# Kernel tuning notes

Hardware: AMD Instinct MI355X
Metric: run time of the kernel (lower is better)

Reference implementation:

```python
import jax, jax.numpy as jnp
import numpy as np

D_MODEL = 1024
D_STATE = 64
D_CONV = 4
EXPAND = 2
HEADDIM = 64
FFN_MULT = 3
MEM_DIM = 256
D_INNER = EXPAND * D_MODEL            # 2048
NHEADS = D_INNER // HEADDIM           # 32
CONV_DIM = D_INNER + 2 * D_STATE      # x, B, C channels through the causal conv
D_IN_PROJ = 2 * D_INNER + 2 * D_STATE + NHEADS  # z, xBC, dt
FFN_HID = FFN_MULT * D_MODEL


def _rms(x, eps=1e-6):
    return x * jax.lax.rsqrt(jnp.mean(x * x, axis=-1, keepdims=True) + eps)


def _mamba2(u, in_proj_w, conv_w, conv_b, dt_bias, A_log, D_param, mnorm_w, out_proj_w):
    # u: [B, L, d_model]
    Bsz, L, _ = u.shape
    zxbcdt = u @ in_proj_w.T                                  # [B, L, D_IN_PROJ]
    z = zxbcdt[..., :D_INNER]                                 # gate branch
    xBC = zxbcdt[..., D_INNER:D_INNER + CONV_DIM]
    dt = zxbcdt[..., D_INNER + CONV_DIM:]                     # [B, L, H]
    # causal depthwise conv1d (kernel D_CONV) + silu
    xp = jnp.pad(xBC, ((0, 0), (D_CONV - 1, 0), (0, 0)))
    xBC = sum(xp[:, k:k + L, :] * conv_w[:, k] for k in range(D_CONV)) + conv_b
    xBC = jax.nn.silu(xBC)
    xh = xBC[..., :D_INNER].reshape(Bsz, L, NHEADS, HEADDIM)  # [B, L, H, P]
    Bm = xBC[..., D_INNER:D_INNER + D_STATE]                  # [B, L, N] (ngroups=1)
    Cm = xBC[..., D_INNER + D_STATE:]                         # [B, L, N]
    dt = jax.nn.softplus(dt + dt_bias)                        # [B, L, H]
    dA = jnp.exp(dt * (-jnp.exp(A_log)))                      # [B, L, H]

    def step(h, inp):
        # h: [B, H, P, N]
        da, dtt, xt, bt, ct = inp
        h = da[:, :, None, None] * h + jnp.einsum('bh,bhp,bn->bhpn', dtt, xt, bt)
        y = jnp.einsum('bhpn,bn->bhp', h, ct)
        return h, y

    h0 = jnp.zeros((Bsz, NHEADS, HEADDIM, D_STATE), u.dtype)
    xs = (jnp.moveaxis(dA, 1, 0), jnp.moveaxis(dt, 1, 0), jnp.moveaxis(xh, 1, 0),
          jnp.moveaxis(Bm, 1, 0), jnp.moveaxis(Cm, 1, 0))
    _, ys = jax.lax.scan(step, h0, xs)                        # ys: [L, B, H, P]
    y = jnp.moveaxis(ys, 0, 1) + D_param[None, None, :, None] * xh
    y = y.reshape(Bsz, L, D_INNER)
    y = _rms(y * jax.nn.silu(z)) * mnorm_w                    # RMSNormGated
    return y @ out_proj_w.T


def setup_inputs() -> dict:
    key = jax.random.key(0)
    ks = jax.random.split(key, 12)
    B, L = 1, 2048
    s = 0.02
    return {
        'x': jax.random.normal(ks[0], (B, L, D_MODEL), jnp.float32),
        'x0': jax.random.normal(ks[1], (B, L, D_MODEL), jnp.float32),
        'mem': jax.random.normal(ks[2], (B, MEM_DIM), jnp.float32),
        'resid_mix': jnp.stack([jnp.ones(D_MODEL), jnp.zeros(D_MODEL)]),
        'ssm_scale': jnp.ones(D_MODEL),
        'mlp_scale': jnp.ones(D_MODEL),
        'ssm_norm_w': jnp.ones(D_MODEL),
        'ffn_norm_w': jnp.ones(D_MODEL),
        'in_proj_w': jax.random.normal(ks[3], (D_IN_PROJ, D_MODEL), jnp.float32) * s,
        'conv_w': jax.random.normal(ks[4], (CONV_DIM, D_CONV), jnp.float32) * 0.2,
        'conv_b': jnp.zeros(CONV_DIM),
        'dt_bias': jax.random.uniform(ks[5], (NHEADS,), jnp.float32, -2.0, 0.0),
        'A_log': jnp.log(jnp.linspace(1.0, 16.0, NHEADS).astype(jnp.float32)),
        'D_param': jnp.ones(NHEADS),
        'mnorm_w': jnp.ones(D_INNER),
        'out_proj_w': jax.random.normal(ks[6], (D_MODEL, D_INNER), jnp.float32) * s,
        'gate_up_w': jax.random.normal(ks[7], (2 * FFN_HID, D_MODEL), jnp.float32) * s,
        'down_w': jax.random.normal(ks[8], (D_MODEL, FFN_HID), jnp.float32) * s,
    }


def reference(x, x0, mem, resid_mix, ssm_scale, mlp_scale, ssm_norm_w, ffn_norm_w,
              in_proj_w, conv_w, conv_b, dt_bias, A_log, D_param, mnorm_w,
              out_proj_w, gate_up_w, down_w):
    # residual mixing (USE_MEMORY=0, so mem path is inert)
    x = resid_mix[0][None, None, :] * x + resid_mix[1][None, None, :] * x0
    y = _mamba2(_rms(x) * ssm_norm_w, in_proj_w, conv_w, conv_b, dt_bias,
                A_log, D_param, mnorm_w, out_proj_w)
    x = x + ssm_scale[None, None, :] * y
    # SwiGLU FFN
    h = _rms(x) * ffn_norm_w
    gu = h @ gate_up_w.T
    gate, up = jnp.split(gu, 2, axis=-1)
    x = x + mlp_scale[None, None, :] * ((jax.nn.silu(gate) * up) @ down_w.T)
    return x
```

## Files before the change

kernel.cpp:

```cpp
#include <hip/hip_runtime.h>
#include <hip/hip_bf16.h>
#include <math.h>

#define LSEQ 2048
#define DMODEL 1024
#define DINNER 2048
#define NHEADS 32
#define HEADDIM 64
#define DSTATE 64
#define CONVDIM 2176
#define XBCDT_W 2304
#define FFNHID 3072

typedef float f32x4 __attribute__((ext_vector_type(4)));
typedef __bf16 bf16x8 __attribute__((ext_vector_type(8)));
typedef __hip_bfloat16 bf16;

__device__ __forceinline__ float siluf(float x){ return x / (1.0f + expf(-x)); }

#define GLOAD_LDS16(gp, lp) __builtin_amdgcn_global_load_lds( \
    (const __attribute__((address_space(1))) void*)(gp), \
    (__attribute__((address_space(3))) void*)(lp), 16, 0, 0)

__device__ __forceinline__ float block_reduce_sum_256(float v){
  #pragma unroll
  for (int o = 32; o > 0; o >>= 1) v += __shfl_down(v, o, 64);
  __shared__ float sh[4];
  int lane = threadIdx.x & 63;
  int w = threadIdx.x >> 6;
  if (lane == 0) sh[w] = v;
  __syncthreads();
  return sh[0] + sh[1] + sh[2] + sh[3];
}

__device__ __forceinline__ ushort bf16bits(float f){
  __hip_bfloat16 h = __float2bfloat16(f);
  return *reinterpret_cast<ushort*>(&h);
}

__device__ __forceinline__ int swz64(int r, int c){
  return r*64 + ((((c>>3) ^ (r&7)))<<3) + (c&7);
}

__global__ __launch_bounds__(256) void k_castmix(
    const float* __restrict__ w0, const float* __restrict__ w1,
    const float* __restrict__ w2, const float* __restrict__ w3,
    bf16* __restrict__ d0, bf16* __restrict__ d1,
    bf16* __restrict__ d2, bf16* __restrict__ d3,
    const float* __restrict__ x, const float* __restrict__ x0,
    const float* __restrict__ rm, const float* __restrict__ nw,
    float* __restrict__ xres, bf16* __restrict__ u)
{
  int tid = threadIdx.x;
  if (blockIdx.x < 15616){
    int idx = blockIdx.x * 256 + tid;
    const float* s; bf16* d; int valid;
    if (idx < 1114112)      { s = w0; d = d0; valid = 1089536; }
    else if (idx < 1638400) { idx -= 1114112; s = w1; d = d1; valid = 524288; }
    else if (idx < 3211264) { idx -= 1638400; s = w2; d = d2; valid = 1572864; }
    else                    { idx -= 3211264; s = w3; d = d3; valid = 786432; }
    float4 v = (idx < valid) ? *(const float4*)(s + (size_t)idx * 4)
                             : make_float4(0.f, 0.f, 0.f, 0.f);
    ushort4 r;
    r.x = bf16bits(v.x); r.y = bf16bits(v.y); r.z = bf16bits(v.z); r.w = bf16bits(v.w);
    *(ushort4*)(d + (size_t)idx * 4) = r;
    return;
  }
  int row = blockIdx.x - 15616;
  float4 xv  = ((const float4*)(x  + (size_t)row * DMODEL))[tid];
  float4 x0v = ((const float4*)(x0 + (size_t)row * DMODEL))[tid];
  float4 r0 = ((const float4*)rm)[tid];
  float4 r1 = ((const float4*)(rm + DMODEL))[tid];
  float4 a;
  a.x = r0.x*xv.x + r1.x*x0v.x; a.y = r0.y*xv.y + r1.y*x0v.y;
  a.z = r0.z*xv.z + r1.z*x0v.z; a.w = r0.w*xv.w + r1.w*x0v.w;
  ((float4*)(xres + (size_t)row * DMODEL))[tid] = a;
  float ss = a.x*a.x + a.y*a.y + a.z*a.z + a.w*a.w;
  ss = block_reduce_sum_256(ss);
  float inv = rsqrtf(ss / (float)DMODEL + 1e-6f);
  float4 nv = ((const float4*)nw)[tid];
  ushort4 o;
  o.x = bf16bits(a.x*inv*nv.x); o.y = bf16bits(a.y*inv*nv.y);
  o.z = bf16bits(a.z*inv*nv.z); o.w = bf16bits(a.w*inv*nv.w);
  *(ushort4*)(u + (size_t)row * DMODEL + tid*4) = o;
}

__device__ __forceinline__ void gemm_mainloop64(
    const bf16* __restrict__ A, const bf16* __restrict__ W,
    int ld, int Klen, bf16* As, bf16* Ws, f32x4 acc[4][2])
{
  int tid = threadIdx.x, lane = tid & 63, wid = tid >> 6;
  int wm = (wid >> 1) * 64, wn = (wid & 1) * 32;
  int r16 = lane & 15, g8 = lane >> 4;
  int srow = lane >> 2;
  int scol = ((lane & 3) ^ (srow & 3)) * 8;
  const bf16* ga0 = A + (size_t)(wid*32 + srow) * ld + scol;
  const bf16* ga1 = ga0 + (size_t)16 * ld;
  const bf16* gw0 = W + (size_t)(wid*16 + srow) * ld + scol;
  GLOAD_LDS16(ga0, As + wid*1024);
  GLOAD_LDS16(ga1, As + wid*1024 + 512);
  GLOAD_LDS16(gw0, Ws + wid*512);
  __syncthreads();
  int cur = 0, s4 = (r16 & 3) * 8;
  for (int k0 = 0; k0 < Klen; k0 += 32){
    if (k0 + 32 < Klen){
      GLOAD_LDS16(ga0 + k0 + 32, As + (cur^1)*4096 + wid*1024);
      GLOAD_LDS16(ga1 + k0 + 32, As + (cur^1)*4096 + wid*1024 + 512);
      GLOAD_LDS16(gw0 + k0 + 32, Ws + (cur^1)*2048 + wid*512);
    }
    const bf16* cA = As + cur*4096;
    const bf16* cW = Ws + cur*2048;
    bf16x8 af[4], bfr[2];
    #pragma unroll
    for (int i = 0; i < 4; ++i)
      af[i] = *(const bf16x8*)(cA + (wm + i*16 + r16)*32 + (g8*8 ^ s4));
    #pragma unroll
    for (int j = 0; j < 2; ++j)
      bfr[j] = *(const bf16x8*)(cW + (wn + j*16 + r16)*32 + (g8*8 ^ s4));
    #pragma unroll
    for (int i = 0; i < 4; ++i)
      #pragma unroll
      for (int j = 0; j < 2; ++j)
        acc[i][j] = __builtin_amdgcn_mfma_f32_16x16x32_bf16(af[i], bfr[j], acc[i][j], 0, 0, 0);
    __syncthreads();
    cur ^= 1;
  }
}

__global__ __launch_bounds__(256) void k_gemm_inproj(
    const bf16* __restrict__ A, const bf16* __restrict__ Wfull,
    float* __restrict__ zbuf, float* __restrict__ xbcdt)
{
  __shared__ __align__(16) bf16 As[2*4096];
  __shared__ __align__(16) bf16 Ws[2*2048];
  int bx = blockIdx.x, by = blockIdx.y;
  f32x4 acc[4][2];
  #pragma unroll
  for (int i = 0; i < 4; ++i)
    #pragma unroll
    for (int j = 0; j < 2; ++j) acc[i][j] = (f32x4){0.f,0.f,0.f,0.f};
  gemm_mainloop64(A + (size_t)(by*128)*DMODEL, Wfull + (size_t)(bx*64)*DMODEL,
                  DMODEL, DMODEL, As, Ws, acc);
  int tid = threadIdx.x, lane = tid & 63, wid = tid >> 6;
  int wm = (wid >> 1) * 64, wn = (wid & 1) * 32;
  int r16 = lane & 15, g8 = lane >> 4;
  float* Cp; int ldc, col0;
  if (bx < 32){ Cp = zbuf;  ldc = DINNER;  col0 = bx*64; }
  else        { Cp = xbcdt; ldc = XBCDT_W; col0 = (bx-32)*64; }
  #pragma unroll
  for (int i = 0; i < 4; ++i){
    int row = by*128 + wm + i*16 + g8*4;
    #pragma unroll
    for (int j = 0; j < 2; ++j){
      int col = col0 + wn + j*16 + r16;
      #pragma unroll
      for (int r = 0; r < 4; ++r)
        Cp[(size_t)(row + r) * ldc + col] = acc[i][j][r];
    }
  }
}

__global__ __launch_bounds__(256) void k_gemm_splitk(
    const bf16* __restrict__ A, const bf16* __restrict__ W,
    float* __restrict__ P, int Kfull, int Khalf, int N)
{
  __shared__ __align__(16) bf16 As[2*4096];
  __shared__ __align__(16) bf16 Ws[2*2048];
  f32x4 acc[4][2];
  #pragma unroll
  for (int i = 0; i < 4; ++i)
    #pragma unroll
    for (int j = 0; j < 2; ++j) acc[i][j] = (f32x4){0.f,0.f,0.f,0.f};
  int z = blockIdx.z;
  gemm_mainloop64(A + (size_t)(blockIdx.y*128)*Kfull + z*Khalf,
                  W + (size_t)(blockIdx.x*64)*Kfull + z*Khalf,
                  Kfull, Khalf, As, Ws, acc);
  float* Pz = P + (size_t)z * LSEQ * N;
  int tid = threadIdx.x, lane = tid & 63, wid = tid >> 6;
  int wm = (wid >> 1) * 64, wn = (wid & 1) * 32;
  int r16 = lane & 15, g8 = lane >> 4;
  #pragma unroll
  for (int i = 0; i < 4; ++i){
    int row = blockIdx.y*128 + wm + i*16 + g8*4;
    #pragma unroll
    for (int j = 0; j < 2; ++j){
      int col = blockIdx.x*64 + wn + j*16 + r16;
      #pragma unroll
      for (int r = 0; r < 4; ++r)
        Pz[(size_t)(row + r) * N + col] = acc[i][j][r];
    }
  }
}

__global__ __launch_bounds__(256) void k_gemm_ffn(
    const bf16* __restrict__ A, const bf16* __restrict__ Wg, const bf16* __restrict__ Wu,
    bf16* __restrict__ act, int K)
{
  __shared__ __align__(16) bf16 As[2*4096];
  __shared__ __align__(16) bf16 Gs[2*2048];
  __shared__ __align__(16) bf16 Us[2*2048];
  int tid = threadIdx.x, lane = tid & 63, wid = tid >> 6;
  int wm = (wid >> 1) * 64, wn = (wid & 1) * 32;
  int r16 = lane & 15, g8 = lane >> 4;
  int srow = lane >> 2;
  int scol = ((lane & 3) ^ (srow & 3)) * 8;
  const bf16* ga0 = A  + (size_t)(blockIdx.y*128 + wid*32 + srow) * K + scol;
  const bf16* ga1 = ga0 + (size_t)16*K;
  const bf16* gg0 = Wg + (size_t)(blockIdx.x*64 + wid*16 + srow) * K + scol;
  const bf16* gu0 = Wu + (size_t)(blockIdx.x*64 + wid*16 + srow) * K + scol;
  f32x4 accg[4][2], accu[4][2];
  #pragma unroll
  for (int i = 0; i < 4; ++i)
    #pragma unroll
    for (int j = 0; j < 2; ++j){
      accg[i][j] = (f32x4){0.f,0.f,0.f,0.f};
      accu[i][j] = (f32x4){0.f,0.f,0.f,0.f};
    }
  GLOAD_LDS16(ga0, As + wid*1024);
  GLOAD_LDS16(ga1, As + wid*1024 + 512);
  GLOAD_LDS16(gg0, Gs + wid*512);
  GLOAD_LDS16(gu0, Us + wid*512);
  __syncthreads();
  int cur = 0, s4 = (r16 & 3) * 8;
  for (int k0 = 0; k0 < K; k0 += 32){
    if (k0 + 32 < K){
      GLOAD_LDS16(ga0 + k0 + 32, As + (cur^1)*4096 + wid*1024);
      GLOAD_LDS16(ga1 + k0 + 32, As + (cur^1)*4096 + wid*1024 + 512);
      GLOAD_LDS16(gg0 + k0 + 32, Gs + (cur^1)*2048 + wid*512);
      GLOAD_LDS16(gu0 + k0 + 32, Us + (cur^1)*2048 + wid*512);
    }
    const bf16* cA = As + cur*4096;
    const bf16* cG = Gs + cur*2048;
    const bf16* cU = Us + cur*2048;
    bf16x8 af[4], gf[2], uf[2];
    #pragma unroll
    for (int i = 0; i < 4; ++i)
      af[i] = *(const bf16x8*)(cA + (wm + i*16 + r16)*32 + (g8*8 ^ s4));
    #pragma unroll
    for (int j = 0; j < 2; ++j){
      gf[j] = *(const bf16x8*)(cG + (wn + j*16 + r16)*32 + (g8*8 ^ s4));
      uf[j] = *(const bf16x8*)(cU + (wn + j*16 + r16)*32 + (g8*8 ^ s4));
    }
    #pragma unroll
    for (int i = 0; i < 4; ++i)
      #pragma unroll
      for (int j = 0; j < 2; ++j){
        accg[i][j] = __builtin_amdgcn_mfma_f32_16x16x32_bf16(af[i], gf[j], accg[i][j], 0, 0, 0);
        accu[i][j] = __builtin_amdgcn_mfma_f32_16x16x32_bf16(af[i], uf[j], accu[i][j], 0, 0, 0);
      }
    __syncthreads();
    cur ^= 1;
  }
  #pragma unroll
  for (int i = 0; i < 4; ++i){
    int row = blockIdx.y*128 + wm + i*16 + g8*4;
    #pragma unroll
    for (int j = 0; j < 2; ++j){
      int col = blockIdx.x*64 + wn + j*16 + r16;
      #pragma unroll
      for (int r = 0; r < 4; ++r){
        float g = accg[i][j][r], u = accu[i][j][r];
        act[(size_t)(row + r) * FFNHID + col] = __float2bfloat16(siluf(g) * u);
      }
    }
  }
}

__global__ __launch_bounds__(256) void k_convdt(
    const float* __restrict__ xbcdt, const float* __restrict__ cw,
    const float* __restrict__ cb, const float* __restrict__ dtb,
    const float* __restrict__ alog, float* __restrict__ xbc,
    float* __restrict__ dtv, float* __restrict__ lav)
{
  int idx = blockIdx.x * 256 + threadIdx.x;
  if (idx >= LSEQ * 2208) return;
  int l = idx / 2208, c = idx - l * 2208;
  if (c < CONVDIM){
    float acc = cb[c];
    #pragma unroll
    for (int k = 0; k < 4; ++k){
      int t = l + k - 3;
      if (t >= 0) acc = fmaf(xbcdt[(size_t)t * XBCDT_W + c], cw[c*4 + k], acc);
    }
    xbc[(size_t)l * CONVDIM + c] = siluf(acc);
  } else {
    int h = c - CONVDIM;
    float raw = xbcdt[(size_t)l * XBCDT_W + c] + dtb[h];
    float d = (raw > 20.f) ? raw : log1pf(expf(raw));
    dtv[l * NHEADS + h] = d;
    lav[l * NHEADS + h] = -expf(alog[h]) * d;
  }
}

__global__ __launch_bounds__(256) void k_scanA(
    const float* __restrict__ xbc, const float* __restrict__ dtv,
    const float* __restrict__ lav, float* __restrict__ T, float* __restrict__ ctot)
{
  __shared__ bf16 sXw[4096];
  __shared__ bf16 sBt[4096];
  __shared__ float scum[64], swt[64];
  int h = blockIdx.x >> 5, c = blockIdx.x & 31;
  int tid = threadIdx.x, t0 = c * 64;
  if (tid < 64){
    float cum = lav[(size_t)(t0 + tid) * NHEADS + h];
    #pragma unroll
    for (int o = 1; o < 64; o <<= 1){
      float v = __shfl_up(cum, o, 64);
      if (tid >= o) cum += v;
    }
    scum[tid] = cum;
  }
  __syncthreads();
  float Lc = scum[63];
  if (tid < 64)
    swt[tid] = expf(Lc - scum[tid]) * dtv[(size_t)(t0 + tid) * NHEADS + h];
  __syncthreads();
  for (int idx = tid; idx < 4096; idx += 256){
    int j = idx >> 6, n = idx & 63;
    size_t rb = (size_t)(t0 + j) * CONVDIM;
    sXw[swz64(n, j)] = __float2bfloat16(xbc[rb + h * HEADDIM + n] * swt[j]);
    sBt[swz64(n, j)] = __float2bfloat16(xbc[rb + DINNER + n]);
  }
  __syncthreads();
  int lane = tid & 63, wid = tid >> 6;
  int wr = (wid >> 1) * 32, wc = (wid & 1) * 32;
  int r16 = lane & 15, g8 = lane >> 4;
  f32x4 acc[2][2];
  #pragma unroll
  for (int i = 0; i < 2; ++i)
    #pragma unroll
    for (int j = 0; j < 2; ++j) acc[i][j] = (f32x4){0.f,0.f,0.f,0.f};
  #pragma unroll
  for (int kk = 0; kk < 2; ++kk){
    int ks = kk*4 + g8;
    bf16x8 a[2], b[2];
    #pragma unroll
    for (int i = 0; i < 2; ++i){
      int row = wr + i*16 + r16;
      a[i] = *(const bf16x8*)(sXw + row*64 + ((ks ^ (row&7))<<3));
    }
    #pragma unroll
    for (int j = 0; j < 2; ++j){
      int row = wc + j*16 + r16;
      b[j] = *(const bf16x8*)(sBt + row*64 + ((ks ^ (row&7))<<3));
    }
    #pragma unroll
    for (int i = 0; i < 2; ++i)
      #pragma unroll
      for (int j = 0; j < 2; ++j)
        acc[i][j] = __builtin_amdgcn_mfma_f32_16x16x32_bf16(a[i], b[j], acc[i][j], 0, 0, 0);
  }
  float* Tb = T + (size_t)blockIdx.x * 4096;
  #pragma unroll
  for (int i = 0; i < 2; ++i)
    #pragma unroll
    for (int j = 0; j < 2; ++j)
      #pragma unroll
      for (int r = 0; r < 4; ++r){
        int p = wr + i*16 + g8*4 + r, n = wc + j*16 + r16;
        Tb[p*64 + n] = acc[i][j][r];
      }
  if (tid == 0) ctot[blockIdx.x] = expf(Lc);
}

__global__ __launch_bounds__(256) void k_scanB(float* __restrict__ T, const float* __restrict__ ctot)
{
  int h = blockIdx.x >> 3, e = blockIdx.x & 7;
  int tid = threadIdx.x;
  size_t off = (size_t)e * 512 + tid * 2;
  float s0 = 0.f, s1 = 0.f;
  for (int c = 0; c < 32; ++c){
    float ct = ctot[h * 32 + c];
    size_t base = (size_t)(h * 32 + c) * 4096 + off;
    float2 tv = *(const float2*)&T[base];
    *(float2*)&T[base] = make_float2(s0, s1);
    s0 = fmaf(ct, s0, tv.x);
    s1 = fmaf(ct, s1, tv.y);
  }
}

__global__ __launch_bounds__(256) void k_scanC(
    const float* __restrict__ xbc, const float* __restrict__ Sin,
    const float* __restrict__ dtv, const float* __restrict__ lav,
    const float* __restrict__ Dp, float* __restrict__ y)
{
  __shared__ bf16 sC[4096];
  __shared__ bf16 sBS[4096];
  __shared__ bf16 sXt[4096];
  __shared__ bf16 sXr[4096];
  __shared__ bf16 sSb[4096];
  __shared__ float scum[64], sdt[64];
  int h = blockIdx.x >> 5, c = blockIdx.x & 31;
  int tid = threadIdx.x, t0 = c * 64;
  if (tid < 64){
    float cum = lav[(size_t)(t0 + tid) * NHEADS + h];
    #pragma unroll
    for (int o = 1; o < 64; o <<= 1){
      float v = __shfl_up(cum, o, 64);
      if (tid >= o) cum += v;
    }
    scum[tid] = cum;
    sdt[tid] = dtv[(size_t)(t0 + tid) * NHEADS + h];
  }
  for (int idx = tid; idx < 4096; idx += 256){
    int j = idx >> 6, n = idx & 63;
    size_t rb = (size_t)(t0 + j) * CONVDIM;
    float xv = xbc[rb + h * HEADDIM + n];
    sC [swz64(j, n)] = __float2bfloat16(xbc[rb + DINNER + DSTATE + n]);
    sBS[swz64(j, n)] = __float2bfloat16(xbc[rb + DINNER + n]);
    sXr[swz64(j, n)] = __float2bfloat16(xv);
    sXt[swz64(n, j)] = __float2bfloat16(xv);
    sSb[swz64(j, n)] = __float2bfloat16(Sin[(size_t)blockIdx.x * 4096 + idx]);
  }
  __syncthreads();
  int lane = tid & 63, wid = tid >> 6;
  int wr = (wid >> 1) * 32, wc = (wid & 1) * 32;
  int r16 = lane & 15, g8 = lane >> 4;
  f32x4 gacc[2][2];
  #pragma unroll
  for (int i = 0; i < 2; ++i)
    #pragma unroll
    for (int j = 0; j < 2; ++j) gacc[i][j] = (f32x4){0.f,0.f,0.f,0.f};
  #pragma unroll
  for (int kk = 0; kk < 2; ++kk){
    int ks = kk*4 + g8;
    bf16x8 a[2], b[2];
    #pragma unroll
    for (int i = 0; i < 2; ++i){
      int row = wr + i*16 + r16;
      a[i] = *(const bf16x8*)(sC + row*64 + ((ks ^ (row&7))<<3));
    }
    #pragma unroll
    for (int j = 0; j < 2; ++j){
      int row = wc + j*16 + r16;
      b[j] = *(const bf16x8*)(sBS + row*64 + ((ks ^ (row&7))<<3));
    }
    #pragma unroll
    for (int i = 0; i < 2; ++i)
      #pragma unroll
      for (int j = 0; j < 2; ++j)
        gacc[i][j] = __builtin_amdgcn_mfma_f32_16x16x32_bf16(a[i], b[j], gacc[i][j], 0, 0, 0);
  }
  __syncthreads();
  #pragma unroll
  for (int i = 0; i < 2; ++i)
    #pragma unroll
    for (int j = 0; j < 2; ++j)
      #pragma unroll
      for (int r = 0; r < 4; ++r){
        int i_ = wr + i*16 + g8*4 + r, j_ = wc + j*16 + r16;
        float v = (j_ <= i_) ? gacc[i][j][r] * expf(scum[i_] - scum[j_]) * sdt[j_] : 0.f;
        sBS[swz64(i_, j_)] = __float2bfloat16(v);
      }
  __syncthreads();
  f32x4 a1[2][2], a2[2][2];
  #pragma unroll
  for (int i = 0; i < 2; ++i)
    #pragma unroll
    for (int j = 0; j < 2; ++j){
      a1[i][j] = (f32x4){0.f,0.f,0.f,0.f};
      a2[i][j] = (f32x4){0.f,0.f,0.f,0.f};
    }
  #pragma unroll
  for (int kk = 0; kk < 2; ++kk){
    int ks = kk*4 + g8;
    bf16x8 sa[2], xa[2], ca[2], sb[2];
    #pragma unroll
    for (int i = 0; i < 2; ++i){
      int row = wr + i*16 + r16;
      sa[i] = *(const bf16x8*)(sBS + row*64 + ((ks ^ (row&7))<<3));
      ca[i] = *(const bf16x8*)(sC  + row*64 + ((ks ^ (row&7))<<3));
    }
    #pragma unroll
    for (int j = 0; j < 2; ++j){
      int row = wc + j*16 + r16;
      xa[j] = *(const bf16x8*)(sXt + row*64 + ((ks ^ (row&7))<<3));
      sb[j] = *(const bf16x8*)(sSb + row*64 + ((ks ^ (row&7))<<3));
    }
    #pragma unroll
    for (int i = 0; i < 2; ++i)
      #pragma unroll
      for (int j = 0; j < 2; ++j){
        a1[i][j] = __builtin_amdgcn_mfma_f32_16x16x32_bf16(sa[i], xa[j], a1[i][j], 0, 0, 0);
        a2[i][j] = __builtin_amdgcn_mfma_f32_16x16x32_bf16(ca[i], sb[j], a2[i][j], 0, 0, 0);
      }
  }
  float Dh = Dp[h];
  #pragma unroll
  for (int i = 0; i < 2; ++i)
    #pragma unroll
    for (int r = 0; r < 4; ++r){
      int i_ = wr + i*16 + g8*4 + r;
      float wi = expf(scum[i_]);
      #pragma unroll
      for (int j = 0; j < 2; ++j){
        int p_ = wc + j*16 + r16;
        float xv = __bfloat162float(sXr[swz64(i_, p_)]);
        y[(size_t)(t0 + i_) * DINNER + h * HEADDIM + p_] =
            a1[i][j][r] + wi * a2[i][j][r] + Dh * xv;
      }
    }
}

__global__ __launch_bounds__(256) void k_gate_rms(
    const float* __restrict__ y, const float* __restrict__ zbuf,
    const float* __restrict__ mw, bf16* __restrict__ yn)
{
  int row = blockIdx.x, tid = threadIdx.x;
  const float4* yr = (const float4*)(y    + (size_t)row * DINNER);
  const float4* zr = (const float4*)(zbuf + (size_t)row * DINNER);
  float4 v[2]; float ss = 0.f;
  #pragma unroll
  for (int i = 0; i < 2; ++i){
    int d4 = tid + i * 256;
    float4 yv = yr[d4], zv = zr[d4];
    float4 g;
    g.x = yv.x * siluf(zv.x); g.y = yv.y * siluf(zv.y);
    g.z = yv.z * siluf(zv.z); g.w = yv.w * siluf(zv.w);
    v[i] = g;
    ss += g.x*g.x + g.y*g.y + g.z*g.z + g.w*g.w;
  }
  ss = block_reduce_sum_256(ss);
  float inv = rsqrtf(ss / (float)DINNER + 1e-6f);
  #pragma unroll
  for (int i = 0; i < 2; ++i){
    int d4 = tid + i * 256;
    float4 mv = ((const float4*)mw)[d4];
    ushort4 o;
    o.x = bf16bits(v[i].x*inv*mv.x); o.y = bf16bits(v[i].y*inv*mv.y);
    o.z = bf16bits(v[i].z*inv*mv.z); o.w = bf16bits(v[i].w*inv*mv.w);
    *(ushort4*)(yn + (size_t)row * DINNER + d4*4) = o;
  }
}

__global__ __launch_bounds__(256) void k_res_rms(
    const float* __restrict__ xres, const float* __restrict__ yo0,
    const float* __restrict__ yo1, const float* __restrict__ scale,
    const float* __restrict__ nw, float* __restrict__ x2, bf16* __restrict__ hb)
{
  int row = blockIdx.x, tid = threadIdx.x;
  float4 xv = ((const float4*)(xres + (size_t)row * DMODEL))[tid];
  float4 y0 = ((const float4*)(yo0  + (size_t)row * DMODEL))[tid];
  float4 y1 = ((const float4*)(yo1  + (size_t)row * DMODEL))[tid];
  float4 sv = ((const float4*)scale)[tid];
  float4 a;
  a.x = xv.x + sv.x*(y0.x+y1.x); a.y = xv.y + sv.y*(y0.y+y1.y);
  a.z = xv.z + sv.z*(y0.z+y1.z); a.w = xv.w + sv.w*(y0.w+y1.w);
  ((float4*)(x2 + (size_t)row * DMODEL))[tid] = a;
  float ss = a.x*a.x + a.y*a.y + a.z*a.z + a.w*a.w;
  ss = block_reduce_sum_256(ss);
  float inv = rsqrtf(ss / (float)DMODEL + 1e-6f);
  float4 nv = ((const float4*)nw)[tid];
  ushort4 o;
  o.x = bf16bits(a.x*inv*nv.x); o.y = bf16bits(a.y*inv*nv.y);
  o.z = bf16bits(a.z*inv*nv.z); o.w = bf16bits(a.w*inv*nv.w);
  *(ushort4*)(hb + (size_t)row * DMODEL + tid*4) = o;
}

__global__ __launch_bounds__(256) void k_final(
    const float* __restrict__ x2, const float* __restrict__ d0,
    const float* __restrict__ d1, const float* __restrict__ mscale,
    float* __restrict__ out)
{
  int i4 = blockIdx.x * 256 + threadIdx.x;
  float4 xv = ((const float4*)x2)[i4];
  float4 a  = ((const float4*)d0)[i4];
  float4 b  = ((const float4*)d1)[i4];
  float4 mv = ((const float4*)mscale)[i4 & 255];
  float4 o;
  o.x = xv.x + mv.x*(a.x+b.x); o.y = xv.y + mv.y*(a.y+b.y);
  o.z = xv.z + mv.z*(a.z+b.z); o.w = xv.w + mv.w*(a.w+b.w);
  ((float4*)out)[i4] = o;
}

extern "C" void kernel_launch(void* const* d_in, const int* in_sizes, int n_in,
                              void* d_out, int out_size, void* d_ws, size_t ws_size,
                              hipStream_t stream)
{
  const float* x      = (const float*)d_in[0];
  const float* x0     = (const float*)d_in[1];
  const float* rm     = (const float*)d_in[3];
  const float* sscale = (const float*)d_in[4];
  const float* mscale = (const float*)d_in[5];
  const float* snw    = (const float*)d_in[6];
  const float* fnw    = (const float*)d_in[7];
  const float* win    = (const float*)d_in[8];
  const float* cw     = (const float*)d_in[9];
  const float* cb     = (const float*)d_in[10];
  const float* dtb    = (const float*)d_in[11];
  const float* alog   = (const float*)d_in[12];
  const float* Dp     = (const float*)d_in[13];
  const float* mnw    = (const float*)d_in[14];
  const float* wout   = (const float*)d_in[15];
  const float* wgu    = (const float*)d_in[16];
  const float* wdn    = (const float*)d_in[17];
  float* out = (float*)d_out;

  const size_t MB = 1024ull * 1024ull;
  char* ws = (char*)d_ws;
  bf16*  winb  = (bf16*) (ws + 0*MB);
  bf16*  act   = (bf16*) (ws + 0*MB);
  bf16*  woutb = (bf16*) (ws + 13*MB);
  bf16*  wgub  = (bf16*) (ws + 17*MB);
  bf16*  wdnb  = (bf16*) (ws + 29*MB);
  float* xres  = (float*)(ws + 35*MB);
  bf16*  u     = (bf16*) (ws + 43*MB);
  float* dtv   = (float*)(ws + 43*MB);
  float* lav   = (float*)(ws + 43*MB + 256*1024);
  bf16*  hb    = (bf16*) (ws + 43*MB);
  float* zbuf  = (float*)(ws + 47*MB);
  float* x2    = (float*)(ws + 47*MB);
  float* dP    = (float*)(ws + 55*MB);
  float* xbcdt = (float*)(ws + 63*MB);
  float* yb    = (float*)(ws + 63*MB);
  float* xbc   = (float*)(ws + 81*MB);
  float* yoP   = (float*)(ws + 81*MB);
  float* T     = (float*)(ws + 98*MB);
  bf16*  yn    = (bf16*) (ws + 98*MB);
  float* ctot  = (float*)(ws + 114*MB);

  dim3 blk(256);
  k_castmix<<<17664, blk, 0, stream>>>(win, wout, wgu, wdn, winb, woutb, wgub, wdnb,
                                       x, x0, rm, snw, xres, u);
  k_gemm_inproj<<<dim3(68,16), blk, 0, stream>>>(u, winb, zbuf, xbcdt);
  k_convdt<<<(LSEQ*2208 + 255)/256, blk, 0, stream>>>(xbcdt, cw, cb, dtb, alog, xbc, dtv, lav);
  k_scanA<<<NHEADS*32, blk, 0, stream>>>(xbc, dtv, lav, T, ctot);
  k_scanB<<<NHEADS*8, blk, 0, stream>>>(T, ctot);
  k_scanC<<<NHEADS*32, blk, 0, stream>>>(xbc, T, dtv, lav, Dp, yb);
  k_gate_rms<<<LSEQ, blk, 0, stream>>>(yb, zbuf, mnw, yn);
  k_gemm_splitk<<<dim3(16,16,2), blk, 0, stream>>>(yn, woutb, yoP, DINNER, DINNER/2, DMODEL);
  k_res_rms<<<LSEQ, blk, 0, stream>>>(xres, yoP, yoP + (size_t)LSEQ*DMODEL, sscale, fnw, x2, hb);
  k_gemm_ffn<<<dim3(48,16), blk, 0, stream>>>(hb, wgub, wgub + (size_t)FFNHID*DMODEL, act, DMODEL);
  k_gemm_splitk<<<dim3(16,16,2), blk, 0, stream>>>(act, wdnb, dP, FFNHID, FFNHID/2, DMODEL);
  k_final<<<2048, blk, 0, stream>>>(x2, dP, dP + (size_t)LSEQ*DMODEL, mscale, out);
}
```

Measured before the change: 224.0 us.

## Triple-buffer GEMM LDS pipeline with one barrier per K-step and MFMA priority

```diff
diff --git a/kernel.cpp b/kernel.cpp
--- a/kernel.cpp
+++ b/kernel.cpp
@@ -85,7 +85,7 @@
   *(ushort4*)(u + (size_t)row * DMODEL + tid*4) = o;
 }
 
-__device__ __forceinline__ void gemm_mainloop64(
+__device__ __forceinline__ void gemm_mainloop64_p2(
     const bf16* __restrict__ A, const bf16* __restrict__ W,
     int ld, int Klen, bf16* As, bf16* Ws, f32x4 acc[4][2])
 {
@@ -97,16 +97,28 @@
   const bf16* ga0 = A + (size_t)(wid*32 + srow) * ld + scol;
   const bf16* ga1 = ga0 + (size_t)16 * ld;
   const bf16* gw0 = W + (size_t)(wid*16 + srow) * ld + scol;
+  int nk = Klen >> 5;
   GLOAD_LDS16(ga0, As + wid*1024);
   GLOAD_LDS16(ga1, As + wid*1024 + 512);
   GLOAD_LDS16(gw0, Ws + wid*512);
-  __syncthreads();
-  int cur = 0, s4 = (r16 & 3) * 8;
-  for (int k0 = 0; k0 < Klen; k0 += 32){
-    if (k0 + 32 < Klen){
-      GLOAD_LDS16(ga0 + k0 + 32, As + (cur^1)*4096 + wid*1024);
-      GLOAD_LDS16(ga1 + k0 + 32, As + (cur^1)*4096 + wid*1024 + 512);
-      GLOAD_LDS16(gw0 + k0 + 32, Ws + (cur^1)*2048 + wid*512);
+  if (nk > 1){
+    GLOAD_LDS16(ga0 + 32, As + 4096 + wid*1024);
+    GLOAD_LDS16(ga1 + 32, As + 4096 + wid*1024 + 512);
+    GLOAD_LDS16(gw0 + 32, Ws + 2048 + wid*512);
+  }
+  int s4 = (r16 & 3) * 8;
+  for (int ks = 0; ks < nk; ++ks){
+    int cur = ks % 3;
+    if (ks + 1 < nk) asm volatile("s_waitcnt vmcnt(3)" ::: "memory");
+    else             asm volatile("s_waitcnt vmcnt(0)" ::: "memory");
+    __builtin_amdgcn_s_barrier();
+    __builtin_amdgcn_sched_barrier(0);
+    int k2 = (ks + 2) << 5;
+    if (k2 < Klen){
+      int nb = (ks + 2) % 3;
+      GLOAD_LDS16(ga0 + k2, As + nb*4096 + wid*1024);
+      GLOAD_LDS16(ga1 + k2, As + nb*4096 + wid*1024 + 512);
+      GLOAD_LDS16(gw0 + k2, Ws + nb*2048 + wid*512);
     }
     const bf16* cA = As + cur*4096;
     const bf16* cW = Ws + cur*2048;
@@ -117,13 +129,13 @@
     #pragma unroll
     for (int j = 0; j < 2; ++j)
       bfr[j] = *(const bf16x8*)(cW + (wn + j*16 + r16)*32 + (g8*8 ^ s4));
+    __builtin_amdgcn_s_setprio(1);
     #pragma unroll
     for (int i = 0; i < 4; ++i)
       #pragma unroll
       for (int j = 0; j < 2; ++j)
         acc[i][j] = __builtin_amdgcn_mfma_f32_16x16x32_bf16(af[i], bfr[j], acc[i][j], 0, 0, 0);
-    __syncthreads();
-    cur ^= 1;
+    __builtin_amdgcn_s_setprio(0);
   }
 }
 
@@ -131,16 +143,16 @@
     const bf16* __restrict__ A, const bf16* __restrict__ Wfull,
     float* __restrict__ zbuf, float* __restrict__ xbcdt)
 {
-  __shared__ __align__(16) bf16 As[2*4096];
-  __shared__ __align__(16) bf16 Ws[2*2048];
+  __shared__ __align__(16) bf16 As[3*4096];
+  __shared__ __align__(16) bf16 Ws[3*2048];
   int bx = blockIdx.x, by = blockIdx.y;
   f32x4 acc[4][2];
   #pragma unroll
   for (int i = 0; i < 4; ++i)
     #pragma unroll
     for (int j = 0; j < 2; ++j) acc[i][j] = (f32x4){0.f,0.f,0.f,0.f};
-  gemm_mainloop64(A + (size_t)(by*128)*DMODEL, Wfull + (size_t)(bx*64)*DMODEL,
-                  DMODEL, DMODEL, As, Ws, acc);
+  gemm_mainloop64_p2(A + (size_t)(by*128)*DMODEL, Wfull + (size_t)(bx*64)*DMODEL,
+                     DMODEL, DMODEL, As, Ws, acc);
   int tid = threadIdx.x, lane = tid & 63, wid = tid >> 6;
   int wm = (wid >> 1) * 64, wn = (wid & 1) * 32;
   int r16 = lane & 15, g8 = lane >> 4;
@@ -164,17 +176,17 @@
     const bf16* __restrict__ A, const bf16* __restrict__ W,
     float* __restrict__ P, int Kfull, int Khalf, int N)
 {
-  __shared__ __align__(16) bf16 As[2*4096];
-  __shared__ __align__(16) bf16 Ws[2*2048];
+  __shared__ __align__(16) bf16 As[3*4096];
+  __shared__ __align__(16) bf16 Ws[3*2048];
   f32x4 acc[4][2];
   #pragma unroll
   for (int i = 0; i < 4; ++i)
     #pragma unroll
     for (int j = 0; j < 2; ++j) acc[i][j] = (f32x4){0.f,0.f,0.f,0.f};
   int z = blockIdx.z;
-  gemm_mainloop64(A + (size_t)(blockIdx.y*128)*Kfull + z*Khalf,
-                  W + (size_t)(blockIdx.x*64)*Kfull + z*Khalf,
-                  Kfull, Khalf, As, Ws, acc);
+  gemm_mainloop64_p2(A + (size_t)(blockIdx.y*128)*Kfull + z*Khalf,
+                     W + (size_t)(blockIdx.x*64)*Kfull + z*Khalf,
+                     Kfull, Khalf, As, Ws, acc);
   float* Pz = P + (size_t)z * LSEQ * N;
   int tid = threadIdx.x, lane = tid & 63, wid = tid >> 6;
   int wm = (wid >> 1) * 64, wn = (wid & 1) * 32;
@@ -196,9 +208,9 @@
     const bf16* __restrict__ A, const bf16* __restrict__ Wg, const bf16* __restrict__ Wu,
     bf16* __restrict__ act, int K)
 {
-  __shared__ __align__(16) bf16 As[2*4096];
-  __shared__ __align__(16) bf16 Gs[2*2048];
-  __shared__ __align__(16) bf16 Us[2*2048];
+  __shared__ __align__(16) bf16 As[3*4096];
+  __shared__ __align__(16) bf16 Gs[3*2048];
+  __shared__ __align__(16) bf16 Us[3*2048];
   int tid = threadIdx.x, lane = tid & 63, wid = tid >> 6;
   int wm = (wid >> 1) * 64, wn = (wid & 1) * 32;
   int r16 = lane & 15, g8 = lane >> 4;
@@ -216,18 +228,31 @@
       accg[i][j] = (f32x4){0.f,0.f,0.f,0.f};
       accu[i][j] = (f32x4){0.f,0.f,0.f,0.f};
     }
+  int nk = K >> 5;
   GLOAD_LDS16(ga0, As + wid*1024);
   GLOAD_LDS16(ga1, As + wid*1024 + 512);
   GLOAD_LDS16(gg0, Gs + wid*512);
   GLOAD_LDS16(gu0, Us + wid*512);
-  __syncthreads();
-  int cur = 0, s4 = (r16 & 3) * 8;
-  for (int k0 = 0; k0 < K; k0 += 32){
-    if (k0 + 32 < K){
-      GLOAD_LDS16(ga0 + k0 + 32, As + (cur^1)*4096 + wid*1024);
-      GLOAD_LDS16(ga1 + k0 + 32, As + (cur^1)*4096 + wid*1024 + 512);
-      GLOAD_LDS16(gg0 + k0 + 32, Gs + (cur^1)*2048 + wid*512);
-      GLOAD_LDS16(gu0 + k0 + 32, Us + (cur^1)*2048 + wid*512);
+  if (nk > 1){
+    GLOAD_LDS16(ga0 + 32, As + 4096 + wid*1024);
+    GLOAD_LDS16(ga1 + 32, As + 4096 + wid*1024 + 512);
+    GLOAD_LDS16(gg0 + 32, Gs + 2048 + wid*512);
+    GLOAD_LDS16(gu0 + 32, Us + 2048 + wid*512);
+  }
+  int s4 = (r16 & 3) * 8;
+  for (int ks = 0; ks < nk; ++ks){
+    int cur = ks % 3;
+    if (ks + 1 < nk) asm volatile("s_waitcnt vmcnt(4)" ::: "memory");
+    else             asm volatile("s_waitcnt vmcnt(0)" ::: "memory");
+    __builtin_amdgcn_s_barrier();
+    __builtin_amdgcn_sched_barrier(0);
+    int k2 = (ks + 2) << 5;
+    if (k2 < K){
+      int nb = (ks + 2) % 3;
+      GLOAD_LDS16(ga0 + k2, As + nb*4096 + wid*1024);
+      GLOAD_LDS16(ga1 + k2, As + nb*4096 + wid*1024 + 512);
+      GLOAD_LDS16(gg0 + k2, Gs + nb*2048 + wid*512);
+      GLOAD_LDS16(gu0 + k2, Us + nb*2048 + wid*512);
     }
     const bf16* cA = As + cur*4096;
     const bf16* cG = Gs + cur*2048;
@@ -241,6 +266,7 @@
       gf[j] = *(const bf16x8*)(cG + (wn + j*16 + r16)*32 + (g8*8 ^ s4));
       uf[j] = *(const bf16x8*)(cU + (wn + j*16 + r16)*32 + (g8*8 ^ s4));
     }
+    __builtin_amdgcn_s_setprio(1);
     #pragma unroll
     for (int i = 0; i < 4; ++i)
       #pragma unroll
@@ -248,8 +274,7 @@
         accg[i][j] = __builtin_amdgcn_mfma_f32_16x16x32_bf16(af[i], gf[j], accg[i][j], 0, 0, 0);
         accu[i][j] = __builtin_amdgcn_mfma_f32_16x16x32_bf16(af[i], uf[j], accu[i][j], 0, 0, 0);
       }
-    __syncthreads();
-    cur ^= 1;
+    __builtin_amdgcn_s_setprio(0);
   }
   #pragma unroll
   for (int i = 0; i < 4; ++i){
```

Measured after the change: 242.3 us. 1.08x slower.
